# Optimization experiments

Measured on AMD Instinct MI355X. Metric: run time of the kernel, lower is better.

The kernel has to match this reference:

```python
import jax, jax.numpy as jnp
import numpy as np

B, S, H, F, E, TOPK = 2, 2048, 1024, 512, 8, 2


def setup_inputs() -> dict:
    key = jax.random.key(0)
    k1, k2, k3, k4, k5 = jax.random.split(key, 5)
    s_h = 1.0 / np.sqrt(H)
    s_f = 1.0 / np.sqrt(F)
    return {
        "x": jax.random.normal(k1, (B, S, H), dtype=jnp.float32),
        "Wr": jax.random.normal(k2, (H, E), dtype=jnp.float32) * s_h,   # router
        "Wg": jax.random.normal(k3, (E, H, F), dtype=jnp.float32) * s_h,  # gate proj
        "Wu": jax.random.normal(k4, (E, H, F), dtype=jnp.float32) * s_h,  # up proj
        "Wd": jax.random.normal(k5, (E, F, H), dtype=jnp.float32) * s_f,  # down proj
        "topk": TOPK,
    }


def reference(x, Wr, Wg, Wu, Wd, topk):
    Bq, Sq, Hq = x.shape
    Eq = Wr.shape[1]
    xf = x.reshape(-1, Hq)                      # [T, H]
    logits = xf @ Wr                            # [T, E]
    probs = jax.nn.softmax(logits, axis=-1)
    w, idx = jax.lax.top_k(probs, topk)         # [T, topk]
    w = w / jnp.sum(w, axis=-1, keepdims=True)  # normalize top-k probs (Qwen3-style)
    # combine coefficients per (token, expert): scatter top-k weights
    coeff = jnp.sum(jax.nn.one_hot(idx, Eq, dtype=w.dtype) * w[..., None], axis=1)  # [T, E]
    # dense dispatch/combine (math-equivalent to per-expert gather + scatter-add)
    gate = jnp.einsum('th,ehf->tef', xf, Wg)    # [T, E, F]
    up = jnp.einsum('th,ehf->tef', xf, Wu)
    act = jax.nn.silu(gate) * up                # SwiGLU expert
    # apply combine weight before down-proj (linearity) to avoid a [T,E,H] temp
    out = jnp.einsum('tef,efh->th', act * coeff[:, :, None], Wd)
    return out.reshape(Bq, Sq, Hq)
```

## Files before the change

kernel.cpp:

```cpp
#include <hip/hip_runtime.h>
#include <hip/hip_bf16.h>

#define T_TOK    4096
#define H_DIM    1024
#define F_DIM    512
#define N_EXP    8
#define N_ASSIGN 8192
#define BM 128
#define BN 128
#define BK 64
#define MAX_TILES 80
#define GRID_MT   71

typedef __bf16 bf16x8 __attribute__((ext_vector_type(8)));
typedef __bf16 bf16x2 __attribute__((ext_vector_type(2)));
typedef float  f32x4  __attribute__((ext_vector_type(4)));

#define MFMA16(a, b, c) __builtin_amdgcn_mfma_f32_16x16x32_bf16((a), (b), (c), 0, 0, 0)

__device__ __forceinline__ void gl_lds16(const __bf16* g, __bf16* l) {
    __builtin_amdgcn_global_load_lds(
        (const __attribute__((address_space(1))) unsigned int*)g,
        (__attribute__((address_space(3))) unsigned int*)l,
        16, 0, 0);
}

__global__ __launch_bounds__(256) void routing_kernel(
    const float* __restrict__ x, const float* __restrict__ Wr,
    __bf16* __restrict__ xb, int* __restrict__ top_e, float* __restrict__ top_w)
{
    int wave = threadIdx.x >> 6, lane = threadIdx.x & 63;
    int t = blockIdx.x * 4 + wave;
    const float* xrow = x + (size_t)t * H_DIM;
    __bf16* xbrow = xb + (size_t)t * H_DIM;

    float part[N_EXP];
#pragma unroll
    for (int e = 0; e < N_EXP; ++e) part[e] = 0.f;

#pragma unroll
    for (int half = 0; half < 2; ++half) {
        int h0 = half * 512 + lane * 8;
        float4 v0 = *(const float4*)(xrow + h0);
        float4 v1 = *(const float4*)(xrow + h0 + 4);
        float xs[8] = {v0.x, v0.y, v0.z, v0.w, v1.x, v1.y, v1.z, v1.w};
        bf16x8 bv;
#pragma unroll
        for (int i = 0; i < 8; ++i) bv[i] = (__bf16)xs[i];
        *(bf16x8*)(xbrow + h0) = bv;
#pragma unroll
        for (int i = 0; i < 8; ++i) {
            const float4* wr = (const float4*)(Wr + (size_t)(h0 + i) * N_EXP);
            float4 w0 = wr[0], w1 = wr[1];
            part[0] += xs[i] * w0.x; part[1] += xs[i] * w0.y;
            part[2] += xs[i] * w0.z; part[3] += xs[i] * w0.w;
            part[4] += xs[i] * w1.x; part[5] += xs[i] * w1.y;
            part[6] += xs[i] * w1.z; part[7] += xs[i] * w1.w;
        }
    }
#pragma unroll
    for (int m = 1; m < 64; m <<= 1) {
#pragma unroll
        for (int e = 0; e < N_EXP; ++e) part[e] += __shfl_xor(part[e], m, 64);
    }
    if (lane == 0) {
        float v1 = -1e30f, v2 = -1e30f;
        int i1 = 0, i2 = 0;
#pragma unroll
        for (int e = 0; e < N_EXP; ++e) {
            float p = part[e];
            if (p > v1)      { v2 = v1; i2 = i1; v1 = p; i1 = e; }
            else if (p > v2) { v2 = p;  i2 = e; }
        }
        float w1 = 1.f / (1.f + __expf(v2 - v1));
        top_e[t * 2]     = i1;  top_e[t * 2 + 1] = i2;
        top_w[t * 2]     = w1;  top_w[t * 2 + 1] = 1.f - w1;
    }
}

__global__ __launch_bounds__(256) void scan_kernel(
    const int* __restrict__ top_e,
    int* __restrict__ tile_e, int* __restrict__ tile_m0, int* __restrict__ tile_cnt,
    int* __restrict__ n_tiles, int* __restrict__ tbase)
{
    __shared__ int hist[N_EXP][256];
    __shared__ int ebase[N_EXP];
    int tid = threadIdx.x;

    int c[N_EXP];
#pragma unroll
    for (int e = 0; e < N_EXP; ++e) c[e] = 0;
#pragma unroll 4
    for (int i = 0; i < 32; ++i) {
        int ee = top_e[tid * 32 + i];
#pragma unroll
        for (int e = 0; e < N_EXP; ++e) c[e] += (ee == e);
    }
#pragma unroll
    for (int e = 0; e < N_EXP; ++e) hist[e][tid] = c[e];
    __syncthreads();

    for (int s = 1; s < 256; s <<= 1) {
        int v[N_EXP];
#pragma unroll
        for (int e = 0; e < N_EXP; ++e) v[e] = (tid >= s) ? hist[e][tid - s] : 0;
        __syncthreads();
#pragma unroll
        for (int e = 0; e < N_EXP; ++e) hist[e][tid] += v[e];
        __syncthreads();
    }

    if (tid == 0) {
        int o = 0, nt = 0;
        for (int e = 0; e < N_EXP; ++e) {
            ebase[e] = o;
            int ne = hist[e][255];
            for (int m0 = 0; m0 < ne; m0 += BM) {
                tile_e[nt]   = e;
                tile_m0[nt]  = o + m0;
                tile_cnt[nt] = (ne - m0 < BM) ? (ne - m0) : BM;
                ++nt;
            }
            o += ne;
        }
        *n_tiles = nt;
    }
    __syncthreads();

#pragma unroll
    for (int e = 0; e < N_EXP; ++e)
        tbase[e * 256 + tid] = ebase[e] + hist[e][tid] - c[e];
}

__global__ __launch_bounds__(256) void scatter_kernel(
    const int* __restrict__ top_e, const float* __restrict__ top_w,
    const int* __restrict__ tbase,
    int* __restrict__ perm, float* __restrict__ wts)
{
    int e = blockIdx.x, tid = threadIdx.x;
    int base = tbase[e * 256 + tid];
#pragma unroll 4
    for (int i = 0; i < 32; ++i) {
        int a = tid * 32 + i;
        if (top_e[a] == e) {
            perm[base] = a >> 1;
            wts[base]  = top_w[a];
            ++base;
        }
    }
}

__global__ __launch_bounds__(256) void transpose_kernel(
    const float* __restrict__ Wg, const float* __restrict__ Wu, const float* __restrict__ Wd,
    __bf16* __restrict__ Wcat, __bf16* __restrict__ Wdt)
{
    int z = blockIdx.z;
    const float* src; int R, C;
    if (z < 8)       { src = Wg + (size_t)z * H_DIM * F_DIM;        R = H_DIM; C = F_DIM; }
    else if (z < 16) { src = Wu + (size_t)(z - 8) * H_DIM * F_DIM;  R = H_DIM; C = F_DIM; }
    else             { src = Wd + (size_t)(z - 16) * F_DIM * H_DIM; R = F_DIM; C = H_DIM; }
    int c0 = blockIdx.x * 32, r0 = blockIdx.y * 64;
    if (c0 >= C || r0 >= R) return;
    __shared__ float tile[64][33];
    int tx = threadIdx.x & 31, ty = threadIdx.x >> 5;
#pragma unroll
    for (int i = 0; i < 8; ++i)
        tile[ty + 8 * i][tx] = src[(size_t)(r0 + ty + 8 * i) * C + c0 + tx];
    __syncthreads();
    if (z < 16) {
        int e = (z < 8) ? z : z - 8;
        int sel = (z < 8) ? 0 : 16;
        __bf16* dst = Wcat + (size_t)e * (2 * F_DIM) * H_DIM;
#pragma unroll
        for (int i = 0; i < 4; ++i) {
            int f = c0 + ty + 8 * i;
            int p = ((f >> 4) << 5) + (f & 15) + sel;
            bf16x2 v = { (__bf16)tile[2 * tx][ty + 8 * i], (__bf16)tile[2 * tx + 1][ty + 8 * i] };
            *(bf16x2*)&dst[(size_t)p * H_DIM + r0 + 2 * tx] = v;
        }
    } else {
        __bf16* dst = Wdt + (size_t)(z - 16) * H_DIM * F_DIM;
#pragma unroll
        for (int i = 0; i < 4; ++i) {
            bf16x2 v = { (__bf16)tile[2 * tx][ty + 8 * i], (__bf16)tile[2 * tx + 1][ty + 8 * i] };
            *(bf16x2*)&dst[(size_t)(c0 + ty + 8 * i) * F_DIM + r0 + 2 * tx] = v;
        }
    }
}

__global__ __launch_bounds__(256, 3) void gateup_kernel(
    const __bf16* __restrict__ xb, const __bf16* __restrict__ Wcat,
    const int* __restrict__ perm, const float* __restrict__ wts,
    const int* __restrict__ tile_e, const int* __restrict__ tile_m0, const int* __restrict__ tile_cnt,
    const int* __restrict__ n_tiles, __bf16* __restrict__ act)
{
    int mt = blockIdx.x >> 3;
    if (mt >= *n_tiles) return;
    int e = tile_e[mt], m0 = tile_m0[mt], mcnt = tile_cnt[mt];
    int n0 = (blockIdx.x & 7) * BN;

    __shared__ __align__(16) __bf16 As[BM * BK];
    __shared__ __align__(16) __bf16 Bs[BN * BK];
    __shared__ int   rowtok[BM];
    __shared__ float roww[BM];

    int tid = threadIdx.x;
    if (tid < BM) {
        int slot = m0 + ((tid < mcnt) ? tid : 0);
        rowtok[tid] = perm[slot];
        roww[tid]   = wts[slot];
    }
    __syncthreads();

    int wave = tid >> 6, lane = tid & 63;
    int srow   = wave * 8 + (lane >> 3);
    int schunk = (((lane & 7) ^ ((lane >> 3) & 7))) * 8;
    const __bf16* We = Wcat + (size_t)e * (2 * F_DIM) * H_DIM;
    const __bf16* aptr[4];
    const __bf16* bptr[4];
#pragma unroll
    for (int j = 0; j < 4; ++j) {
        int r = j * 32 + srow;
        aptr[j] = xb + (size_t)rowtok[r] * H_DIM + schunk;
        bptr[j] = We + (size_t)(n0 + r) * H_DIM + schunk;
    }
    __bf16* aLds = As + wave * 512;
    __bf16* bLds = Bs + wave * 512;

    int wm = wave & 1, wn = wave >> 1;
    int quad = lane >> 4, l16 = lane & 15;

    f32x4 acc[4][4];
#pragma unroll
    for (int a = 0; a < 4; ++a)
#pragma unroll
        for (int b = 0; b < 4; ++b) acc[a][b] = (f32x4){0.f, 0.f, 0.f, 0.f};

    for (int k0 = 0; k0 < H_DIM; k0 += BK) {
#pragma unroll
        for (int j = 0; j < 4; ++j) {
            gl_lds16(aptr[j] + k0, aLds + j * 2048);
            gl_lds16(bptr[j] + k0, bLds + j * 2048);
        }
        __syncthreads();
#pragma unroll
        for (int s = 0; s < 2; ++s) {
            int sw = (((quad + s * 4) ^ (l16 & 7))) * 8;
            bf16x8 af[4], bf[4];
#pragma unroll
            for (int im = 0; im < 4; ++im)
                af[im] = *(const bf16x8*)&As[(wm * 64 + im * 16 + l16) * 64 + sw];
#pragma unroll
            for (int in = 0; in < 4; ++in)
                bf[in] = *(const bf16x8*)&Bs[(wn * 64 + in * 16 + l16) * 64 + sw];
#pragma unroll
            for (int im = 0; im < 4; ++im)
#pragma unroll
                for (int in = 0; in < 4; ++in)
                    acc[im][in] = MFMA16(af[im], bf[in], acc[im][in]);
        }
        __syncthreads();
    }

    int fbase = (n0 >> 1) + wn * 32;
#pragma unroll
    for (int im = 0; im < 4; ++im) {
#pragma unroll
        for (int ip = 0; ip < 2; ++ip) {
            f32x4 g = acc[im][ip * 2], u = acc[im][ip * 2 + 1];
            int fcol = fbase + ip * 16 + l16;
#pragma unroll
            for (int r = 0; r < 4; ++r) {
                int rl = wm * 64 + im * 16 + quad * 4 + r;
                if (rl < mcnt) {
                    float gv = g[r], uv = u[r];
                    float sg = gv / (1.f + __expf(-gv));
                    act[(size_t)(m0 + rl) * F_DIM + fcol] = (__bf16)(sg * uv * roww[rl]);
                }
            }
        }
    }
}

__global__ __launch_bounds__(256, 3) void down_kernel(
    const __bf16* __restrict__ act, const __bf16* __restrict__ Wdt,
    const int* __restrict__ perm,
    const int* __restrict__ tile_e, const int* __restrict__ tile_m0, const int* __restrict__ tile_cnt,
    const int* __restrict__ n_tiles, float* __restrict__ out)
{
    int mt = blockIdx.x >> 3;
    if (mt >= *n_tiles) return;
    int e = tile_e[mt], m0 = tile_m0[mt], mcnt = tile_cnt[mt];
    int n0 = (blockIdx.x & 7) * BN;

    __shared__ __align__(16) __bf16 As[BM * BK];
    __shared__ __align__(16) __bf16 Bs[BN * BK];
    __shared__ int rowtok[BM];

    int tid = threadIdx.x;
    if (tid < BM) rowtok[tid] = perm[m0 + ((tid < mcnt) ? tid : 0)];
    __syncthreads();

    int wave = tid >> 6, lane = tid & 63;
    int srow   = wave * 8 + (lane >> 3);
    int schunk = (((lane & 7) ^ ((lane >> 3) & 7))) * 8;
    const __bf16* Wd_e = Wdt + (size_t)e * H_DIM * F_DIM;
    const __bf16* aptr[4];
    const __bf16* bptr[4];
#pragma unroll
    for (int j = 0; j < 4; ++j) {
        int r = j * 32 + srow;
        int ar = m0 + ((r < mcnt) ? r : 0);
        aptr[j] = act  + (size_t)ar * F_DIM + schunk;
        bptr[j] = Wd_e + (size_t)(n0 + r) * F_DIM + schunk;
    }
    __bf16* aLds = As + wave * 512;
    __bf16* bLds = Bs + wave * 512;

    int wm = wave & 1, wn = wave >> 1;
    int quad = lane >> 4, l16 = lane & 15;

    f32x4 acc[4][4];
#pragma unroll
    for (int a = 0; a < 4; ++a)
#pragma unroll
        for (int b = 0; b < 4; ++b) acc[a][b] = (f32x4){0.f, 0.f, 0.f, 0.f};

    for (int k0 = 0; k0 < F_DIM; k0 += BK) {
#pragma unroll
        for (int j = 0; j < 4; ++j) {
            gl_lds16(aptr[j] + k0, aLds + j * 2048);
            gl_lds16(bptr[j] + k0, bLds + j * 2048);
        }
        __syncthreads();
#pragma unroll
        for (int s = 0; s < 2; ++s) {
            int sw = (((quad + s * 4) ^ (l16 & 7))) * 8;
            bf16x8 af[4], bf[4];
#pragma unroll
            for (int im = 0; im < 4; ++im)
                af[im] = *(const bf16x8*)&As[(wm * 64 + im * 16 + l16) * 64 + sw];
#pragma unroll
            for (int in = 0; in < 4; ++in)
                bf[in] = *(const bf16x8*)&Bs[(wn * 64 + in * 16 + l16) * 64 + sw];
#pragma unroll
            for (int im = 0; im < 4; ++im)
#pragma unroll
                for (int in = 0; in < 4; ++in)
                    acc[im][in] = MFMA16(af[im], bf[in], acc[im][in]);
        }
        __syncthreads();
    }

#pragma unroll
    for (int im = 0; im < 4; ++im) {
#pragma unroll
        for (int in = 0; in < 4; ++in) {
            int col = n0 + wn * 64 + in * 16 + l16;
#pragma unroll
            for (int r = 0; r < 4; ++r) {
                int rl = wm * 64 + im * 16 + quad * 4 + r;
                if (rl < mcnt)
                    unsafeAtomicAdd(out + (size_t)rowtok[rl] * H_DIM + col, acc[im][in][r]);
            }
        }
    }
}

extern "C" void kernel_launch(void* const* d_in, const int* in_sizes, int n_in,
                              void* d_out, int out_size, void* d_ws, size_t ws_size,
                              hipStream_t stream)
{
    const float* x  = (const float*)d_in[0];
    const float* Wr = (const float*)d_in[1];
    const float* Wg = (const float*)d_in[2];
    const float* Wu = (const float*)d_in[3];
    const float* Wd = (const float*)d_in[4];
    float* out = (float*)d_out;

    char* ws = (char*)d_ws;
    size_t off = 0;
    auto carve = [&](size_t bytes) {
        char* p = ws + off;
        off = (off + bytes + 255) & ~(size_t)255;
        return p;
    };
    __bf16* xb   = (__bf16*)carve((size_t)T_TOK * H_DIM * 2);
    __bf16* Wcat = (__bf16*)carve((size_t)N_EXP * 2 * F_DIM * H_DIM * 2);
    __bf16* Wdt  = (__bf16*)carve((size_t)N_EXP * H_DIM * F_DIM * 2);
    __bf16* act  = (__bf16*)carve((size_t)N_ASSIGN * F_DIM * 2);
    int*   top_e = (int*)carve((size_t)T_TOK * 2 * sizeof(int));
    float* top_w = (float*)carve((size_t)T_TOK * 2 * sizeof(float));
    int*   perm  = (int*)carve((size_t)N_ASSIGN * sizeof(int));
    float* wts   = (float*)carve((size_t)N_ASSIGN * sizeof(float));
    int*   tbase = (int*)carve((size_t)N_EXP * 256 * sizeof(int));
    int*   tl_e  = (int*)carve(MAX_TILES * sizeof(int));
    int*   tl_m0 = (int*)carve(MAX_TILES * sizeof(int));
    int*   tl_cn = (int*)carve(MAX_TILES * sizeof(int));
    int*   n_til = (int*)carve(sizeof(int));

    hipMemsetAsync(d_out, 0, (size_t)out_size * sizeof(float), stream);

    routing_kernel<<<T_TOK / 4, 256, 0, stream>>>(x, Wr, xb, top_e, top_w);
    scan_kernel<<<1, 256, 0, stream>>>(top_e, tl_e, tl_m0, tl_cn, n_til, tbase);
    scatter_kernel<<<N_EXP, 256, 0, stream>>>(top_e, top_w, tbase, perm, wts);
    transpose_kernel<<<dim3(32, 16, 24), 256, 0, stream>>>(Wg, Wu, Wd, Wcat, Wdt);
    gateup_kernel<<<GRID_MT * 8, 256, 0, stream>>>(
        xb, Wcat, perm, wts, tl_e, tl_m0, tl_cn, n_til, act);
    down_kernel<<<GRID_MT * 8, 256, 0, stream>>>(
        act, Wdt, perm, tl_e, tl_m0, tl_cn, n_til, out);
}
```

Measured before the change: 221.2 us.

## Replace atomic scatter-add in down projection with partial buffer and combine kernel

The down-projection kernel now writes each assignment's output row to a dense fp32 partial buffer instead of atomically adding into the token output. A new combine kernel sums the two expert partials per token using a token-to-slot map recorded during scatter, and the output memset is dropped. This is meant to remove atomic contention and the memset, at the cost of a 32 MB write plus read and one extra kernel launch. Correctness relies on every token having exactly two distinct expert slots.

```diff
diff --git a/kernel.cpp b/kernel.cpp
--- a/kernel.cpp
+++ b/kernel.cpp
@@ -135,7 +135,7 @@
 __global__ __launch_bounds__(256) void scatter_kernel(
     const int* __restrict__ top_e, const float* __restrict__ top_w,
     const int* __restrict__ tbase,
-    int* __restrict__ perm, float* __restrict__ wts)
+    int* __restrict__ perm, float* __restrict__ wts, int* __restrict__ tokslot)
 {
     int e = blockIdx.x, tid = threadIdx.x;
     int base = tbase[e * 256 + tid];
@@ -143,8 +143,9 @@
     for (int i = 0; i < 32; ++i) {
         int a = tid * 32 + i;
         if (top_e[a] == e) {
-            perm[base] = a >> 1;
-            wts[base]  = top_w[a];
+            perm[base]   = a >> 1;
+            wts[base]    = top_w[a];
+            tokslot[a]   = base;
             ++base;
         }
     }
@@ -284,9 +285,8 @@
 
 __global__ __launch_bounds__(256, 3) void down_kernel(
     const __bf16* __restrict__ act, const __bf16* __restrict__ Wdt,
-    const int* __restrict__ perm,
     const int* __restrict__ tile_e, const int* __restrict__ tile_m0, const int* __restrict__ tile_cnt,
-    const int* __restrict__ n_tiles, float* __restrict__ out)
+    const int* __restrict__ n_tiles, float* __restrict__ P)
 {
     int mt = blockIdx.x >> 3;
     if (mt >= *n_tiles) return;
@@ -295,12 +295,8 @@
 
     __shared__ __align__(16) __bf16 As[BM * BK];
     __shared__ __align__(16) __bf16 Bs[BN * BK];
-    __shared__ int rowtok[BM];
 
     int tid = threadIdx.x;
-    if (tid < BM) rowtok[tid] = perm[m0 + ((tid < mcnt) ? tid : 0)];
-    __syncthreads();
-
     int wave = tid >> 6, lane = tid & 63;
     int srow   = wave * 8 + (lane >> 3);
     int schunk = (((lane & 7) ^ ((lane >> 3) & 7))) * 8;
@@ -361,9 +357,27 @@
             for (int r = 0; r < 4; ++r) {
                 int rl = wm * 64 + im * 16 + quad * 4 + r;
                 if (rl < mcnt)
-                    unsafeAtomicAdd(out + (size_t)rowtok[rl] * H_DIM + col, acc[im][in][r]);
+                    P[(size_t)(m0 + rl) * H_DIM + col] = acc[im][in][r];
             }
         }
+    }
+}
+
+__global__ __launch_bounds__(256) void combine_kernel(
+    const float* __restrict__ P, const int* __restrict__ tokslot,
+    float* __restrict__ out)
+{
+    int wave = threadIdx.x >> 6, lane = threadIdx.x & 63;
+    int t = blockIdx.x * 4 + wave;
+    int s1 = tokslot[2 * t], s2 = tokslot[2 * t + 1];
+    const f32x4* p1 = (const f32x4*)(P + (size_t)s1 * H_DIM);
+    const f32x4* p2 = (const f32x4*)(P + (size_t)s2 * H_DIM);
+    f32x4* o = (f32x4*)(out + (size_t)t * H_DIM);
+#pragma unroll
+    for (int i = 0; i < H_DIM / 4 / 64; ++i) {
+        int idx = i * 64 + lane;
+        f32x4 a = p1[idx], b = p2[idx];
+        o[idx] = (f32x4){a.x + b.x, a.y + b.y, a.z + b.z, a.w + b.w};
     }
 }
 
@@ -389,24 +403,25 @@
     __bf16* Wcat = (__bf16*)carve((size_t)N_EXP * 2 * F_DIM * H_DIM * 2);
     __bf16* Wdt  = (__bf16*)carve((size_t)N_EXP * H_DIM * F_DIM * 2);
     __bf16* act  = (__bf16*)carve((size_t)N_ASSIGN * F_DIM * 2);
+    float* P     = (float*)carve((size_t)N_ASSIGN * H_DIM * sizeof(float));
     int*   top_e = (int*)carve((size_t)T_TOK * 2 * sizeof(int));
     float* top_w = (float*)carve((size_t)T_TOK * 2 * sizeof(float));
     int*   perm  = (int*)carve((size_t)N_ASSIGN * sizeof(int));
     float* wts   = (float*)carve((size_t)N_ASSIGN * sizeof(float));
+    int*  tokslot= (int*)carve((size_t)N_ASSIGN * sizeof(int));
     int*   tbase = (int*)carve((size_t)N_EXP * 256 * sizeof(int));
     int*   tl_e  = (int*)carve(MAX_TILES * sizeof(int));
     int*   tl_m0 = (int*)carve(MAX_TILES * sizeof(int));
     int*   tl_cn = (int*)carve(MAX_TILES * sizeof(int));
     int*   n_til = (int*)carve(sizeof(int));
 
-    hipMemsetAsync(d_out, 0, (size_t)out_size * sizeof(float), stream);
-
     routing_kernel<<<T_TOK / 4, 256, 0, stream>>>(x, Wr, xb, top_e, top_w);
     scan_kernel<<<1, 256, 0, stream>>>(top_e, tl_e, tl_m0, tl_cn, n_til, tbase);
-    scatter_kernel<<<N_EXP, 256, 0, stream>>>(top_e, top_w, tbase, perm, wts);
+    scatter_kernel<<<N_EXP, 256, 0, stream>>>(top_e, top_w, tbase, perm, wts, tokslot);
     transpose_kernel<<<dim3(32, 16, 24), 256, 0, stream>>>(Wg, Wu, Wd, Wcat, Wdt);
     gateup_kernel<<<GRID_MT * 8, 256, 0, stream>>>(
         xb, Wcat, perm, wts, tl_e, tl_m0, tl_cn, n_til, act);
     down_kernel<<<GRID_MT * 8, 256, 0, stream>>>(
-        act, Wdt, perm, tl_e, tl_m0, tl_cn, n_til, out);
-}
+        act, Wdt, tl_e, tl_m0, tl_cn, n_til, P);
+    combine_kernel<<<T_TOK / 4, 256, 0, stream>>>(P, tokslot, out);
+}
```

Result: faster. 206.1 us (-6.8%).
